# Performance work log

Measured on AMD Instinct MI355X. Metric: run time of the kernel, lower is better.

The kernel has to match this reference:

```python
import jax, jax.numpy as jnp
import numpy as np

IMG_SIZE = 1280
STRIDE = 4
NUM_CLASSES = 80
TOPK = 1000
NMS_THRESH = 0.6
SCALE_CLAMP = float(np.log(1000.0))  # DEFAULT_SCALE_CLAMP
N_ANCHORS = (IMG_SIZE // STRIDE) ** 2  # 102400


def _anchors():
    # generate_anchors: meshgrid over fmp, stacked as (x, y), flattened
    fmp = IMG_SIZE // STRIDE
    ys, xs = jnp.meshgrid(jnp.arange(fmp), jnp.arange(fmp), indexing='ij')
    return jnp.stack([xs, ys], axis=-1).reshape(-1, 2).astype(jnp.float32)


def _decode_boxes(anchors, reg):
    # [wl, ht, wr, hb] -> [x1, y1, x2, y2], scaled by stride
    reg = jnp.exp(jnp.minimum(reg, SCALE_CLAMP))
    xy1 = anchors - reg[..., :2]
    xy2 = anchors + reg[..., 2:]
    return jnp.concatenate([xy1, xy2], axis=-1) * STRIDE


def _iou_matrix(b):
    # pairwise IoU with the exact eps handling of the original numpy NMS
    x1, y1, x2, y2 = b[:, 0], b[:, 1], b[:, 2], b[:, 3]
    areas = (x2 - x1) * (y2 - y1)
    xx1 = jnp.maximum(x1[:, None], x1[None, :])
    yy1 = jnp.maximum(y1[:, None], y1[None, :])
    xx2 = jnp.minimum(x2[:, None], x2[None, :])
    yy2 = jnp.minimum(y2[:, None], y2[None, :])
    w = jnp.maximum(1e-10, xx2 - xx1)
    h = jnp.maximum(1e-10, yy2 - yy1)
    inter = w * h
    return inter / (areas[:, None] + areas[None, :] - inter + 1e-10)


def _greedy_nms(iou, same_class):
    # boxes are pre-sorted by score descending (top_k output order), so a
    # single greedy pass with a same-class mask is equivalent to the
    # original per-class loop (each class subset preserves score order).
    K = iou.shape[0]
    suppress = (iou > NMS_THRESH) & same_class
    idx = jnp.arange(K)

    def body(keep, i):
        row = suppress[i] & keep[i]  # only a kept box suppresses others
        keep = keep & ~(row & (idx > i))
        return keep, None

    keep0 = jnp.ones((K,), dtype=bool)
    keep, _ = jax.lax.scan(body, keep0, idx)
    return keep


def setup_inputs() -> dict:
    key = jax.random.key(0)
    k1, k2, k3 = jax.random.split(key, 3)
    hmp_pred = jax.random.normal(k1, (N_ANCHORS, NUM_CLASSES), dtype=jnp.float32)
    reg_pred = jax.random.normal(k2, (N_ANCHORS, 4), dtype=jnp.float32)
    iou_pred = jax.random.normal(k3, (N_ANCHORS, 1), dtype=jnp.float32)
    return {"hmp_pred": hmp_pred, "reg_pred": reg_pred, "iou_pred": iou_pred}


def reference(hmp_pred, reg_pred, iou_pred):
    # score fusion: sqrt(sigmoid(hmp) * sigmoid(iou)), max over classes
    fused = jnp.sqrt(jax.nn.sigmoid(hmp_pred) * jax.nn.sigmoid(iou_pred))  # [N, C]
    scores = jnp.max(fused, axis=-1)
    labels = jnp.argmax(fused, axis=-1)

    # top-k selection (sorted descending)
    scores, indices = jax.lax.top_k(scores, TOPK)
    labels = labels[indices]
    reg = reg_pred[indices]
    anc = _anchors()[indices]

    # decode + normalize + clamp
    bboxes = jnp.clip(_decode_boxes(anc, reg) / IMG_SIZE, 0.0, 1.0)  # [K, 4]

    # class-aware greedy NMS; keep mask replaces the dynamic-shape filter
    same_class = labels[:, None] == labels[None, :]
    keep = _greedy_nms(_iou_matrix(bboxes), same_class)
    return scores, labels, bboxes, keep
```

## Files before the change

kernel.cpp:

```cpp
#include <hip/hip_runtime.h>
#include <stdint.h>

#define N_ANCH 102400
#define FMP 320
#define K_TOP 1000
#define NMS_T 0.6f
#define SC_CLAMP 6.907755278982137f
#define IMGF 1280.0f
#define NBINS 16384

#define OFF_SCORES   0u
#define OFF_LABELS   409600u
#define OFF_HIST     819200u
#define OFF_META     884736u
#define OFF_KEYS     884992u
#define OFF_BOXES    917760u
#define OFF_LAB1K    933760u
#define OFF_MASK     937760u
#define OFF_DIAG     1065760u

__device__ __forceinline__ float sigf(float x) {
    return 1.0f / (1.0f + expf(-x));
}

__global__ __launch_bounds__(256) void k_scores(const float* __restrict__ hmp,
                                                const float* __restrict__ iou,
                                                float* __restrict__ scores,
                                                uint32_t* __restrict__ labels,
                                                uint32_t* __restrict__ hist,
                                                uint32_t* __restrict__ meta,
                                                uint64_t* __restrict__ diag) {
    int blk = blockIdx.x;
    if (blk < 64) {
        hist[blk * 256 + threadIdx.x] = 0u;
    } else if (blk == 64) {
        if (threadIdx.x < 64) meta[threadIdx.x] = 0u;
#pragma unroll
        for (int k = 0; k < 4; ++k) diag[threadIdx.x * 4 + k] = 0ull;
    }
    int gid = blk * 256 + threadIdx.x;
    int a = gid >> 2;
    int q = gid & 3;
    float si = sigf(iou[a]);
    const float4* row4 = (const float4*)hmp + (size_t)a * 20 + q;
    float4 v[5];
#pragma unroll
    for (int j = 0; j < 5; ++j) v[j] = row4[j * 4];
    float best = -1.0f;
    int bc = 0;
#pragma unroll
    for (int j = 0; j < 5; ++j) {
        int cb = j * 16 + q * 4;
        float f;
        f = sqrtf(sigf(v[j].x) * si); if (f > best) { best = f; bc = cb; }
        f = sqrtf(sigf(v[j].y) * si); if (f > best) { best = f; bc = cb + 1; }
        f = sqrtf(sigf(v[j].z) * si); if (f > best) { best = f; bc = cb + 2; }
        f = sqrtf(sigf(v[j].w) * si); if (f > best) { best = f; bc = cb + 3; }
    }
#pragma unroll
    for (int off = 1; off <= 2; off <<= 1) {
        float of = __shfl_xor(best, off);
        int   oc = __shfl_xor(bc, off);
        if (of > best || (of == best && oc < bc)) { best = of; bc = oc; }
    }
    if (q == 0) {
        scores[a] = best;
        labels[a] = (uint32_t)bc;
    }
}

__global__ __launch_bounds__(1024) void k_hist(const float* __restrict__ scores,
                                               uint32_t* __restrict__ hist,
                                               uint32_t* __restrict__ meta) {
    __shared__ uint32_t lh[NBINS];
    __shared__ int lastFlag;
    for (int i = threadIdx.x; i < NBINS; i += 1024) lh[i] = 0u;
    __syncthreads();
    int base = blockIdx.x * 1600;
    for (int k = threadIdx.x; k < 1600; k += 1024) {
        uint32_t bin = __float_as_uint(scores[base + k]) >> 16;
        atomicAdd(&lh[bin], 1u);
    }
    __syncthreads();
    for (int i = threadIdx.x; i < NBINS; i += 1024) {
        uint32_t c = lh[i];
        if (c) atomicAdd(&hist[i], c);
    }
    __threadfence();
    __syncthreads();
    if (threadIdx.x == 0) lastFlag = (atomicAdd(&meta[8], 1u) == 63u);
    __syncthreads();
    if (!lastFlag) return;
    __threadfence();
    int t = threadIdx.x;
    uint32_t s = 0;
#pragma unroll
    for (int b = 0; b < 16; ++b) s += hist[t * 16 + b];
    lh[t] = s;
    __syncthreads();
    for (int off = 1; off < 1024; off <<= 1) {
        uint32_t v = lh[t] + ((t + off < 1024) ? lh[t + off] : 0u);
        __syncthreads();
        lh[t] = v;
        __syncthreads();
    }
    uint32_t inc   = lh[t];
    uint32_t above = (t < 1023) ? lh[t + 1] : 0u;
    if (above < K_TOP && inc >= K_TOP) {
        uint32_t loc[16];
#pragma unroll
        for (int b = 0; b < 16; ++b) loc[b] = hist[t * 16 + b];
        uint32_t cnt = above;
        for (int b = 15; b >= 0; --b) {
            cnt += loc[b];
            if (cnt >= K_TOP) { meta[0] = (uint32_t)(t * 16 + b); break; }
        }
    }
}

__global__ __launch_bounds__(256) void k_collect(const float* __restrict__ scores,
                                                 uint32_t* __restrict__ meta,
                                                 uint64_t* __restrict__ keys) {
    __shared__ uint32_t cnt, base;
    if (threadIdx.x == 0) cnt = 0u;
    __syncthreads();
    int i = blockIdx.x * 256 + threadIdx.x;
    uint32_t bits = __float_as_uint(scores[i]);
    bool cand = (bits >> 16) >= meta[0];
    uint32_t pos = 0;
    if (cand) pos = atomicAdd(&cnt, 1u);
    __syncthreads();
    if (threadIdx.x == 0 && cnt) base = atomicAdd(&meta[2], cnt);
    __syncthreads();
    if (cand) {
        uint32_t p = base + pos;
        if (p < 4096u)
            keys[p] = ((uint64_t)bits << 32) | (uint64_t)(0xFFFFFFFFu - (uint32_t)i);
    }
}

__global__ __launch_bounds__(1024) void k_rank(const uint64_t* __restrict__ keys,
                                               const uint32_t* __restrict__ meta,
                                               const uint32_t* __restrict__ labels,
                                               const float* __restrict__ reg,
                                               float* __restrict__ out,
                                               float* __restrict__ boxes,
                                               uint32_t* __restrict__ lab1k) {
    __shared__ uint64_t sk[4096];
    uint32_t M = meta[2];
    if (M > 4096u) M = 4096u;
    if ((uint32_t)(blockIdx.x * 16) >= M) return;
    for (uint32_t i = threadIdx.x; i < M; i += 1024) sk[i] = keys[i];
    __syncthreads();
    int lane = threadIdx.x & 63;
    int wg = blockIdx.x * 16 + (threadIdx.x >> 6);
    if ((uint32_t)wg >= M) return;
    uint64_t mykey = sk[wg];
    uint32_t rank = 0;
    for (uint32_t j = lane; j < M; j += 64) rank += (sk[j] > mykey) ? 1u : 0u;
#pragma unroll
    for (int off = 32; off; off >>= 1) rank += __shfl_xor(rank, off);
    if (lane != 0 || rank >= K_TOP) return;
    int t = (int)rank;
    uint32_t sbits = (uint32_t)(mykey >> 32);
    uint32_t idx   = 0xFFFFFFFFu - (uint32_t)(mykey & 0xFFFFFFFFull);
    float score = __uint_as_float(sbits);
    uint32_t lab = labels[idx];
    out[t]         = score;
    out[K_TOP + t] = (float)lab;
    lab1k[t]       = lab;
    float ax = (float)(idx % FMP);
    float ay = (float)(idx / FMP);
    float4 rr = ((const float4*)reg)[idx];
    float e0 = expf(fminf(rr.x, SC_CLAMP));
    float e1 = expf(fminf(rr.y, SC_CLAMP));
    float e2 = expf(fminf(rr.z, SC_CLAMP));
    float e3 = expf(fminf(rr.w, SC_CLAMP));
    float x1 = fminf(fmaxf((ax - e0) * 4.0f / IMGF, 0.0f), 1.0f);
    float y1 = fminf(fmaxf((ay - e1) * 4.0f / IMGF, 0.0f), 1.0f);
    float x2 = fminf(fmaxf((ax + e2) * 4.0f / IMGF, 0.0f), 1.0f);
    float y2 = fminf(fmaxf((ay + e3) * 4.0f / IMGF, 0.0f), 1.0f);
    out[2 * K_TOP + t * 4 + 0] = x1;
    out[2 * K_TOP + t * 4 + 1] = y1;
    out[2 * K_TOP + t * 4 + 2] = x2;
    out[2 * K_TOP + t * 4 + 3] = y2;
    boxes[t * 4 + 0] = x1;
    boxes[t * 4 + 1] = y1;
    boxes[t * 4 + 2] = x2;
    boxes[t * 4 + 3] = y2;
}

__global__ __launch_bounds__(1024) void k_mask(const float* __restrict__ boxes,
                                               const uint32_t* __restrict__ lab1k,
                                               uint64_t* __restrict__ mask,
                                               uint64_t* __restrict__ diag) {
    int r = blockIdx.x * 16 + (threadIdx.x >> 6);
    int lane = threadIdx.x & 63;
    if (r >= K_TOP) return;
    float4 bi = ((const float4*)boxes)[r];
    uint32_t li = lab1k[r];
    float areai = (bi.z - bi.x) * (bi.w - bi.y);
    int iw = r >> 6;
    uint64_t dw = 0ull;
#pragma unroll
    for (int w = 0; w < 16; ++w) {
        int j = w * 64 + lane;
        bool sup = false;
        if (j < K_TOP && j > r) {
            float4 bj = ((const float4*)boxes)[j];
            float areaj = (bj.z - bj.x) * (bj.w - bj.y);
            float xx1 = fmaxf(bi.x, bj.x);
            float yy1 = fmaxf(bi.y, bj.y);
            float xx2 = fminf(bi.z, bj.z);
            float yy2 = fminf(bi.w, bj.w);
            float ww = fmaxf(1e-10f, xx2 - xx1);
            float hh = fmaxf(1e-10f, yy2 - yy1);
            float inter = ww * hh;
            float iouv = inter / (areai + areaj - inter + 1e-10f);
            sup = (iouv > NMS_T) && (li == lab1k[j]);
        }
        unsigned long long m = __ballot(sup);
        if (lane == 0) mask[(size_t)r * 16 + w] = (uint64_t)m;
        if (w == iw) dw = (uint64_t)m;
    }
    if (lane == 0) diag[r] = dw;
}

__global__ __launch_bounds__(64, 1) void k_scan(const uint64_t* __restrict__ mask,
                                                const uint64_t* __restrict__ diag,
                                                float* __restrict__ out) {
    int lane = threadIdx.x;
    int q = lane >> 4, wrd = lane & 15;
    uint64_t remv = 0ull;
    uint64_t dcur = diag[lane];
    for (int g = 0; g < 16; ++g) {
        uint64_t dnxt = (g < 15) ? diag[64 * (g + 1) + lane] : 0ull;
        uint64_t bun[16];
        if (g < 15) {
#pragma unroll
            for (int r4 = 0; r4 < 16; ++r4)
                bun[r4] = mask[(size_t)(64 * g + 4 * r4 + q) * 16 + wrd];
        }
        uint32_t dlo = 0, dhi = 0;
#pragma unroll
        for (int qq = 0; qq < 4; ++qq) {
            dlo |= __builtin_amdgcn_readlane((uint32_t)remv, qq * 16 + g);
            dhi |= __builtin_amdgcn_readlane((uint32_t)(remv >> 32), qq * 16 + g);
        }
        uint64_t D = ((uint64_t)dhi << 32) | dlo;
#pragma unroll
        for (int b = 0; b < 64; ++b) {
            uint32_t tlo = __builtin_amdgcn_readlane((uint32_t)dcur, b);
            uint32_t thi = __builtin_amdgcn_readlane((uint32_t)(dcur >> 32), b);
            uint64_t T = ((uint64_t)thi << 32) | tlo;
            uint64_t sel = ((D >> b) & 1ull) - 1ull;
            D |= T & sel;
        }
        uint64_t keepg = ~D;
        int j = g * 64 + lane;
        if (j < K_TOP) out[6 * K_TOP + j] = (float)((keepg >> lane) & 1ull);
        if (g < 15) {
#pragma unroll
            for (int r4 = 0; r4 < 16; ++r4) {
                uint32_t kb = (uint32_t)(keepg >> (4 * r4 + q)) & 1u;
                uint64_t mm = 0ull - (uint64_t)kb;
                remv |= bun[r4] & mm;
            }
        }
        dcur = dnxt;
    }
}

extern "C" void kernel_launch(void* const* d_in, const int* in_sizes, int n_in,
                              void* d_out, int out_size, void* d_ws, size_t ws_size,
                              hipStream_t stream) {
    const float* hmp = (const float*)d_in[0];
    const float* reg = (const float*)d_in[1];
    const float* iou = (const float*)d_in[2];
    float* out = (float*)d_out;
    char* ws = (char*)d_ws;

    float*    scores = (float*)(ws + OFF_SCORES);
    uint32_t* labels = (uint32_t*)(ws + OFF_LABELS);
    uint32_t* hist   = (uint32_t*)(ws + OFF_HIST);
    uint32_t* meta   = (uint32_t*)(ws + OFF_META);
    uint64_t* keys   = (uint64_t*)(ws + OFF_KEYS);
    float*    boxes  = (float*)(ws + OFF_BOXES);
    uint32_t* lab1k  = (uint32_t*)(ws + OFF_LAB1K);
    uint64_t* mask   = (uint64_t*)(ws + OFF_MASK);
    uint64_t* diag   = (uint64_t*)(ws + OFF_DIAG);

    k_scores<<<dim3(N_ANCH * 4 / 256), dim3(256), 0, stream>>>(hmp, iou, scores, labels, hist, meta, diag);
    k_hist<<<dim3(64), dim3(1024), 0, stream>>>(scores, hist, meta);
    k_collect<<<dim3(N_ANCH / 256), dim3(256), 0, stream>>>(scores, meta, keys);
    k_rank<<<dim3(256), dim3(1024), 0, stream>>>(keys, meta, labels, reg, out, boxes, lab1k);
    k_mask<<<dim3(63), dim3(1024), 0, stream>>>(boxes, lab1k, mask, diag);
    k_scan<<<dim3(1), dim3(64), 0, stream>>>(mask, diag, out);
}
```

Baseline: 156.5 us.

## Fuse histogram, collect, rank, mask and scan into one persistent kernel

Replaces five separate launches (histogram, candidate collect, rank/decode, IoU mask, greedy scan) with a single 100-block persistent kernel. The stages are separated by software grid barriers built on atomic counters in the meta area. Each block computes the score cutoff redundantly from the global histogram, which removes the last-block election step. This aims to cut kernel launch gaps and inter-kernel drain time, at the cost of spin-wait barriers that depend on all 100 blocks being resident at once.

```diff
diff --git a/kernel.cpp b/kernel.cpp
--- a/kernel.cpp
+++ b/kernel.cpp
@@ -8,6 +8,8 @@
 #define SC_CLAMP 6.907755278982137f
 #define IMGF 1280.0f
 #define NBINS 16384
+#define NBLK2 100
+#define NTHR2 1024
 
 #define OFF_SCORES   0u
 #define OFF_LABELS   409600u
@@ -21,6 +23,17 @@
 
 __device__ __forceinline__ float sigf(float x) {
     return 1.0f / (1.0f + expf(-x));
+}
+
+__device__ __forceinline__ void gbar(uint32_t* ctr, uint32_t target) {
+    __threadfence();
+    __syncthreads();
+    if (threadIdx.x == 0) {
+        atomicAdd(ctr, 1u);
+        while (atomicAdd(ctr, 0u) < target) __builtin_amdgcn_s_sleep(10);
+    }
+    __syncthreads();
+    __threadfence();
 }
 
 __global__ __launch_bounds__(256) void k_scores(const float* __restrict__ hmp,
@@ -69,205 +82,198 @@
     }
 }
 
-__global__ __launch_bounds__(1024) void k_hist(const float* __restrict__ scores,
-                                               uint32_t* __restrict__ hist,
-                                               uint32_t* __restrict__ meta) {
-    __shared__ uint32_t lh[NBINS];
-    __shared__ int lastFlag;
-    for (int i = threadIdx.x; i < NBINS; i += 1024) lh[i] = 0u;
-    __syncthreads();
-    int base = blockIdx.x * 1600;
-    for (int k = threadIdx.x; k < 1600; k += 1024) {
-        uint32_t bin = __float_as_uint(scores[base + k]) >> 16;
-        atomicAdd(&lh[bin], 1u);
-    }
-    __syncthreads();
-    for (int i = threadIdx.x; i < NBINS; i += 1024) {
-        uint32_t c = lh[i];
+__global__ __launch_bounds__(NTHR2, 4) void k_mega(const float* __restrict__ scores,
+                                                   const uint32_t* __restrict__ labels,
+                                                   const float* __restrict__ reg,
+                                                   uint32_t* __restrict__ hist,
+                                                   uint32_t* __restrict__ meta,
+                                                   uint64_t* __restrict__ keys,
+                                                   float* __restrict__ boxes,
+                                                   uint32_t* __restrict__ lab1k,
+                                                   uint64_t* __restrict__ mask,
+                                                   uint64_t* __restrict__ diag,
+                                                   float* __restrict__ out) {
+    __shared__ __align__(16) uint32_t sh32[NBINS];
+    uint64_t* sk = (uint64_t*)sh32;
+    const int tid  = threadIdx.x;
+    const int blk  = blockIdx.x;
+    const int gtid = blk * NTHR2 + tid;
+    const int lane = tid & 63;
+    const int wv   = tid >> 6;
+
+    for (int i = tid; i < NBINS; i += NTHR2) sh32[i] = 0u;
+    __syncthreads();
+    uint32_t mybits = __float_as_uint(scores[gtid]);
+    atomicAdd(&sh32[mybits >> 16], 1u);
+    __syncthreads();
+    for (int i = tid; i < NBINS; i += NTHR2) {
+        uint32_t c = sh32[i];
         if (c) atomicAdd(&hist[i], c);
     }
-    __threadfence();
-    __syncthreads();
-    if (threadIdx.x == 0) lastFlag = (atomicAdd(&meta[8], 1u) == 63u);
-    __syncthreads();
-    if (!lastFlag) return;
-    __threadfence();
-    int t = threadIdx.x;
-    uint32_t s = 0;
-#pragma unroll
-    for (int b = 0; b < 16; ++b) s += hist[t * 16 + b];
-    lh[t] = s;
-    __syncthreads();
-    for (int off = 1; off < 1024; off <<= 1) {
-        uint32_t v = lh[t] + ((t + off < 1024) ? lh[t + off] : 0u);
+    gbar(&meta[8], NBLK2);
+
+    {
+        uint32_t s = 0;
+#pragma unroll
+        for (int b = 0; b < 16; ++b) s += hist[tid * 16 + b];
+        sh32[tid] = s;
         __syncthreads();
-        lh[t] = v;
+        for (int off = 1; off < NTHR2; off <<= 1) {
+            uint32_t v = sh32[tid] + ((tid + off < NTHR2) ? sh32[tid + off] : 0u);
+            __syncthreads();
+            sh32[tid] = v;
+            __syncthreads();
+        }
+        uint32_t inc   = sh32[tid];
+        uint32_t above = (tid < NTHR2 - 1) ? sh32[tid + 1] : 0u;
+        if (above < K_TOP && inc >= K_TOP) {
+            uint32_t loc[16];
+#pragma unroll
+            for (int b = 0; b < 16; ++b) loc[b] = hist[tid * 16 + b];
+            uint32_t cnt = above;
+            for (int b = 15; b >= 0; --b) {
+                cnt += loc[b];
+                if (cnt >= K_TOP) { sh32[1025] = (uint32_t)(tid * 16 + b); break; }
+            }
+        }
         __syncthreads();
     }
-    uint32_t inc   = lh[t];
-    uint32_t above = (t < 1023) ? lh[t + 1] : 0u;
-    if (above < K_TOP && inc >= K_TOP) {
-        uint32_t loc[16];
-#pragma unroll
-        for (int b = 0; b < 16; ++b) loc[b] = hist[t * 16 + b];
-        uint32_t cnt = above;
-        for (int b = 15; b >= 0; --b) {
-            cnt += loc[b];
-            if (cnt >= K_TOP) { meta[0] = (uint32_t)(t * 16 + b); break; }
-        }
-    }
-}
-
-__global__ __launch_bounds__(256) void k_collect(const float* __restrict__ scores,
-                                                 uint32_t* __restrict__ meta,
-                                                 uint64_t* __restrict__ keys) {
-    __shared__ uint32_t cnt, base;
-    if (threadIdx.x == 0) cnt = 0u;
-    __syncthreads();
-    int i = blockIdx.x * 256 + threadIdx.x;
-    uint32_t bits = __float_as_uint(scores[i]);
-    bool cand = (bits >> 16) >= meta[0];
+    uint32_t cutoff = sh32[1025];
+    __syncthreads();
+
+    if (tid == 0) sh32[0] = 0u;
+    __syncthreads();
+    bool cand = (mybits >> 16) >= cutoff;
     uint32_t pos = 0;
-    if (cand) pos = atomicAdd(&cnt, 1u);
-    __syncthreads();
-    if (threadIdx.x == 0 && cnt) base = atomicAdd(&meta[2], cnt);
+    if (cand) pos = atomicAdd(&sh32[0], 1u);
+    __syncthreads();
+    if (tid == 0) sh32[1] = sh32[0] ? atomicAdd(&meta[2], sh32[0]) : 0u;
     __syncthreads();
     if (cand) {
-        uint32_t p = base + pos;
+        uint32_t p = sh32[1] + pos;
         if (p < 4096u)
-            keys[p] = ((uint64_t)bits << 32) | (uint64_t)(0xFFFFFFFFu - (uint32_t)i);
-    }
-}
-
-__global__ __launch_bounds__(1024) void k_rank(const uint64_t* __restrict__ keys,
-                                               const uint32_t* __restrict__ meta,
-                                               const uint32_t* __restrict__ labels,
-                                               const float* __restrict__ reg,
-                                               float* __restrict__ out,
-                                               float* __restrict__ boxes,
-                                               uint32_t* __restrict__ lab1k) {
-    __shared__ uint64_t sk[4096];
-    uint32_t M = meta[2];
-    if (M > 4096u) M = 4096u;
-    if ((uint32_t)(blockIdx.x * 16) >= M) return;
-    for (uint32_t i = threadIdx.x; i < M; i += 1024) sk[i] = keys[i];
-    __syncthreads();
-    int lane = threadIdx.x & 63;
-    int wg = blockIdx.x * 16 + (threadIdx.x >> 6);
-    if ((uint32_t)wg >= M) return;
-    uint64_t mykey = sk[wg];
-    uint32_t rank = 0;
-    for (uint32_t j = lane; j < M; j += 64) rank += (sk[j] > mykey) ? 1u : 0u;
-#pragma unroll
-    for (int off = 32; off; off >>= 1) rank += __shfl_xor(rank, off);
-    if (lane != 0 || rank >= K_TOP) return;
-    int t = (int)rank;
-    uint32_t sbits = (uint32_t)(mykey >> 32);
-    uint32_t idx   = 0xFFFFFFFFu - (uint32_t)(mykey & 0xFFFFFFFFull);
-    float score = __uint_as_float(sbits);
-    uint32_t lab = labels[idx];
-    out[t]         = score;
-    out[K_TOP + t] = (float)lab;
-    lab1k[t]       = lab;
-    float ax = (float)(idx % FMP);
-    float ay = (float)(idx / FMP);
-    float4 rr = ((const float4*)reg)[idx];
-    float e0 = expf(fminf(rr.x, SC_CLAMP));
-    float e1 = expf(fminf(rr.y, SC_CLAMP));
-    float e2 = expf(fminf(rr.z, SC_CLAMP));
-    float e3 = expf(fminf(rr.w, SC_CLAMP));
-    float x1 = fminf(fmaxf((ax - e0) * 4.0f / IMGF, 0.0f), 1.0f);
-    float y1 = fminf(fmaxf((ay - e1) * 4.0f / IMGF, 0.0f), 1.0f);
-    float x2 = fminf(fmaxf((ax + e2) * 4.0f / IMGF, 0.0f), 1.0f);
-    float y2 = fminf(fmaxf((ay + e3) * 4.0f / IMGF, 0.0f), 1.0f);
-    out[2 * K_TOP + t * 4 + 0] = x1;
-    out[2 * K_TOP + t * 4 + 1] = y1;
-    out[2 * K_TOP + t * 4 + 2] = x2;
-    out[2 * K_TOP + t * 4 + 3] = y2;
-    boxes[t * 4 + 0] = x1;
-    boxes[t * 4 + 1] = y1;
-    boxes[t * 4 + 2] = x2;
-    boxes[t * 4 + 3] = y2;
-}
-
-__global__ __launch_bounds__(1024) void k_mask(const float* __restrict__ boxes,
-                                               const uint32_t* __restrict__ lab1k,
-                                               uint64_t* __restrict__ mask,
-                                               uint64_t* __restrict__ diag) {
-    int r = blockIdx.x * 16 + (threadIdx.x >> 6);
-    int lane = threadIdx.x & 63;
-    if (r >= K_TOP) return;
-    float4 bi = ((const float4*)boxes)[r];
-    uint32_t li = lab1k[r];
-    float areai = (bi.z - bi.x) * (bi.w - bi.y);
-    int iw = r >> 6;
-    uint64_t dw = 0ull;
-#pragma unroll
-    for (int w = 0; w < 16; ++w) {
-        int j = w * 64 + lane;
-        bool sup = false;
-        if (j < K_TOP && j > r) {
-            float4 bj = ((const float4*)boxes)[j];
-            float areaj = (bj.z - bj.x) * (bj.w - bj.y);
-            float xx1 = fmaxf(bi.x, bj.x);
-            float yy1 = fmaxf(bi.y, bj.y);
-            float xx2 = fminf(bi.z, bj.z);
-            float yy2 = fminf(bi.w, bj.w);
-            float ww = fmaxf(1e-10f, xx2 - xx1);
-            float hh = fmaxf(1e-10f, yy2 - yy1);
-            float inter = ww * hh;
-            float iouv = inter / (areai + areaj - inter + 1e-10f);
-            sup = (iouv > NMS_T) && (li == lab1k[j]);
-        }
-        unsigned long long m = __ballot(sup);
-        if (lane == 0) mask[(size_t)r * 16 + w] = (uint64_t)m;
-        if (w == iw) dw = (uint64_t)m;
-    }
-    if (lane == 0) diag[r] = dw;
-}
-
-__global__ __launch_bounds__(64, 1) void k_scan(const uint64_t* __restrict__ mask,
-                                                const uint64_t* __restrict__ diag,
-                                                float* __restrict__ out) {
-    int lane = threadIdx.x;
-    int q = lane >> 4, wrd = lane & 15;
-    uint64_t remv = 0ull;
-    uint64_t dcur = diag[lane];
-    for (int g = 0; g < 16; ++g) {
-        uint64_t dnxt = (g < 15) ? diag[64 * (g + 1) + lane] : 0ull;
-        uint64_t bun[16];
-        if (g < 15) {
-#pragma unroll
-            for (int r4 = 0; r4 < 16; ++r4)
-                bun[r4] = mask[(size_t)(64 * g + 4 * r4 + q) * 16 + wrd];
-        }
-        uint32_t dlo = 0, dhi = 0;
-#pragma unroll
-        for (int qq = 0; qq < 4; ++qq) {
-            dlo |= __builtin_amdgcn_readlane((uint32_t)remv, qq * 16 + g);
-            dhi |= __builtin_amdgcn_readlane((uint32_t)(remv >> 32), qq * 16 + g);
-        }
-        uint64_t D = ((uint64_t)dhi << 32) | dlo;
-#pragma unroll
-        for (int b = 0; b < 64; ++b) {
-            uint32_t tlo = __builtin_amdgcn_readlane((uint32_t)dcur, b);
-            uint32_t thi = __builtin_amdgcn_readlane((uint32_t)(dcur >> 32), b);
-            uint64_t T = ((uint64_t)thi << 32) | tlo;
-            uint64_t sel = ((D >> b) & 1ull) - 1ull;
-            D |= T & sel;
-        }
-        uint64_t keepg = ~D;
-        int j = g * 64 + lane;
-        if (j < K_TOP) out[6 * K_TOP + j] = (float)((keepg >> lane) & 1ull);
-        if (g < 15) {
-#pragma unroll
-            for (int r4 = 0; r4 < 16; ++r4) {
-                uint32_t kb = (uint32_t)(keepg >> (4 * r4 + q)) & 1u;
-                uint64_t mm = 0ull - (uint64_t)kb;
-                remv |= bun[r4] & mm;
-            }
-        }
-        dcur = dnxt;
+            keys[p] = ((uint64_t)mybits << 32) | (uint64_t)(0xFFFFFFFFu - (uint32_t)gtid);
+    }
+    gbar(&meta[9], NBLK2);
+
+    {
+        uint32_t M = meta[2];
+        if (M > 4096u) M = 4096u;
+        for (uint32_t i = tid; i < M; i += NTHR2) sk[i] = keys[i];
+        __syncthreads();
+        for (uint32_t wg = (uint32_t)(blk * 16 + wv); wg < M; wg += NBLK2 * 16) {
+            uint64_t mykey = sk[wg];
+            uint32_t rank = 0;
+            for (uint32_t j = lane; j < M; j += 64) rank += (sk[j] > mykey) ? 1u : 0u;
+#pragma unroll
+            for (int off = 32; off; off >>= 1) rank += __shfl_xor(rank, off);
+            if (lane == 0 && rank < K_TOP) {
+                int t = (int)rank;
+                uint32_t sbits = (uint32_t)(mykey >> 32);
+                uint32_t idx   = 0xFFFFFFFFu - (uint32_t)(mykey & 0xFFFFFFFFull);
+                float score = __uint_as_float(sbits);
+                uint32_t lab = labels[idx];
+                out[t]         = score;
+                out[K_TOP + t] = (float)lab;
+                lab1k[t]       = lab;
+                float ax = (float)(idx % FMP);
+                float ay = (float)(idx / FMP);
+                float4 rr = ((const float4*)reg)[idx];
+                float e0 = expf(fminf(rr.x, SC_CLAMP));
+                float e1 = expf(fminf(rr.y, SC_CLAMP));
+                float e2 = expf(fminf(rr.z, SC_CLAMP));
+                float e3 = expf(fminf(rr.w, SC_CLAMP));
+                float x1 = fminf(fmaxf((ax - e0) * 4.0f / IMGF, 0.0f), 1.0f);
+                float y1 = fminf(fmaxf((ay - e1) * 4.0f / IMGF, 0.0f), 1.0f);
+                float x2 = fminf(fmaxf((ax + e2) * 4.0f / IMGF, 0.0f), 1.0f);
+                float y2 = fminf(fmaxf((ay + e3) * 4.0f / IMGF, 0.0f), 1.0f);
+                out[2 * K_TOP + t * 4 + 0] = x1;
+                out[2 * K_TOP + t * 4 + 1] = y1;
+                out[2 * K_TOP + t * 4 + 2] = x2;
+                out[2 * K_TOP + t * 4 + 3] = y2;
+                boxes[t * 4 + 0] = x1;
+                boxes[t * 4 + 1] = y1;
+                boxes[t * 4 + 2] = x2;
+                boxes[t * 4 + 3] = y2;
+            }
+        }
+    }
+    gbar(&meta[10], NBLK2);
+
+    {
+        int r = blk * 16 + wv;
+        if (r < K_TOP) {
+            float4 bi = ((const float4*)boxes)[r];
+            uint32_t li = lab1k[r];
+            float areai = (bi.z - bi.x) * (bi.w - bi.y);
+            int iw = r >> 6;
+            uint64_t dw = 0ull;
+#pragma unroll
+            for (int w = 0; w < 16; ++w) {
+                int j = w * 64 + lane;
+                bool sup = false;
+                if (j < K_TOP && j > r) {
+                    float4 bj = ((const float4*)boxes)[j];
+                    float areaj = (bj.z - bj.x) * (bj.w - bj.y);
+                    float xx1 = fmaxf(bi.x, bj.x);
+                    float yy1 = fmaxf(bi.y, bj.y);
+                    float xx2 = fminf(bi.z, bj.z);
+                    float yy2 = fminf(bi.w, bj.w);
+                    float ww = fmaxf(1e-10f, xx2 - xx1);
+                    float hh = fmaxf(1e-10f, yy2 - yy1);
+                    float inter = ww * hh;
+                    float iouv = inter / (areai + areaj - inter + 1e-10f);
+                    sup = (iouv > NMS_T) && (li == lab1k[j]);
+                }
+                unsigned long long m = __ballot(sup);
+                if (lane == 0) mask[(size_t)r * 16 + w] = (uint64_t)m;
+                if (w == iw) dw = (uint64_t)m;
+            }
+            if (lane == 0) diag[r] = dw;
+        }
+    }
+    gbar(&meta[11], NBLK2);
+
+    if (blk == 0 && tid < 64) {
+        int q = lane >> 4, wrd = lane & 15;
+        uint64_t remv = 0ull;
+        uint64_t dcur = diag[lane];
+        for (int g = 0; g < 16; ++g) {
+            uint64_t dnxt = (g < 15) ? diag[64 * (g + 1) + lane] : 0ull;
+            uint64_t bun[16];
+            if (g < 15) {
+#pragma unroll
+                for (int r4 = 0; r4 < 16; ++r4)
+                    bun[r4] = mask[(size_t)(64 * g + 4 * r4 + q) * 16 + wrd];
+            }
+            uint32_t dlo = 0, dhi = 0;
+#pragma unroll
+            for (int qq = 0; qq < 4; ++qq) {
+                dlo |= __builtin_amdgcn_readlane((uint32_t)remv, qq * 16 + g);
+                dhi |= __builtin_amdgcn_readlane((uint32_t)(remv >> 32), qq * 16 + g);
+            }
+            uint64_t D = ((uint64_t)dhi << 32) | dlo;
+#pragma unroll
+            for (int b = 0; b < 64; ++b) {
+                uint32_t tlo = __builtin_amdgcn_readlane((uint32_t)dcur, b);
+                uint32_t thi = __builtin_amdgcn_readlane((uint32_t)(dcur >> 32), b);
+                uint64_t T = ((uint64_t)thi << 32) | tlo;
+                uint64_t sel = ((D >> b) & 1ull) - 1ull;
+                D |= T & sel;
+            }
+            uint64_t keepg = ~D;
+            int j = g * 64 + lane;
+            if (j < K_TOP) out[6 * K_TOP + j] = (float)((keepg >> lane) & 1ull);
+            if (g < 15) {
+#pragma unroll
+                for (int r4 = 0; r4 < 16; ++r4) {
+                    uint32_t kb = (uint32_t)(keepg >> (4 * r4 + q)) & 1u;
+                    uint64_t mm = 0ull - (uint64_t)kb;
+                    remv |= bun[r4] & mm;
+                }
+            }
+            dcur = dnxt;
+        }
     }
 }
 
@@ -291,9 +297,6 @@
     uint64_t* diag   = (uint64_t*)(ws + OFF_DIAG);
 
     k_scores<<<dim3(N_ANCH * 4 / 256), dim3(256), 0, stream>>>(hmp, iou, scores, labels, hist, meta, diag);
-    k_hist<<<dim3(64), dim3(1024), 0, stream>>>(scores, hist, meta);
-    k_collect<<<dim3(N_ANCH / 256), dim3(256), 0, stream>>>(scores, meta, keys);
-    k_rank<<<dim3(256), dim3(1024), 0, stream>>>(keys, meta, labels, reg, out, boxes, lab1k);
-    k_mask<<<dim3(63), dim3(1024), 0, stream>>>(boxes, lab1k, mask, diag);
-    k_scan<<<dim3(1), dim3(64), 0, stream>>>(mask, diag, out);
-}
+    k_mega<<<dim3(NBLK2), dim3(NTHR2), 0, stream>>>(scores, labels, reg, hist, meta,
+                                                    keys, boxes, lab1k, mask, diag, out);
+}
```

Result: slower. 338.8 us (+116.5%).

## Fuse threshold, candidate collection and ranking into last histogram block

Applied to the files above, without the earlier changes.

The histogram kernel's last-finishing block now computes the cutoff, rescans all 102400 scores to gather candidates into shared memory, and ranks them there, replacing the separate collect and rank kernels. This removes two kernel launches and the global keys round trip. In exchange, the collection scan and the O(M^2) ranking run on a single 1024-thread block instead of being spread across hundreds of blocks, so serial work on one CU increases.

```diff
diff --git a/kernel.cpp b/kernel.cpp
--- a/kernel.cpp
+++ b/kernel.cpp
@@ -13,7 +13,6 @@
 #define OFF_LABELS   409600u
 #define OFF_HIST     819200u
 #define OFF_META     884736u
-#define OFF_KEYS     884992u
 #define OFF_BOXES    917760u
 #define OFF_LAB1K    933760u
 #define OFF_MASK     937760u
@@ -70,124 +69,117 @@
 }
 
 __global__ __launch_bounds__(1024) void k_hist(const float* __restrict__ scores,
-                                               uint32_t* __restrict__ hist,
-                                               uint32_t* __restrict__ meta) {
-    __shared__ uint32_t lh[NBINS];
-    __shared__ int lastFlag;
-    for (int i = threadIdx.x; i < NBINS; i += 1024) lh[i] = 0u;
-    __syncthreads();
-    int base = blockIdx.x * 1600;
-    for (int k = threadIdx.x; k < 1600; k += 1024) {
-        uint32_t bin = __float_as_uint(scores[base + k]) >> 16;
-        atomicAdd(&lh[bin], 1u);
-    }
-    __syncthreads();
-    for (int i = threadIdx.x; i < NBINS; i += 1024) {
-        uint32_t c = lh[i];
-        if (c) atomicAdd(&hist[i], c);
-    }
-    __threadfence();
-    __syncthreads();
-    if (threadIdx.x == 0) lastFlag = (atomicAdd(&meta[8], 1u) == 63u);
-    __syncthreads();
-    if (!lastFlag) return;
-    __threadfence();
-    int t = threadIdx.x;
-    uint32_t s = 0;
-#pragma unroll
-    for (int b = 0; b < 16; ++b) s += hist[t * 16 + b];
-    lh[t] = s;
-    __syncthreads();
-    for (int off = 1; off < 1024; off <<= 1) {
-        uint32_t v = lh[t] + ((t + off < 1024) ? lh[t + off] : 0u);
-        __syncthreads();
-        lh[t] = v;
-        __syncthreads();
-    }
-    uint32_t inc   = lh[t];
-    uint32_t above = (t < 1023) ? lh[t + 1] : 0u;
-    if (above < K_TOP && inc >= K_TOP) {
-        uint32_t loc[16];
-#pragma unroll
-        for (int b = 0; b < 16; ++b) loc[b] = hist[t * 16 + b];
-        uint32_t cnt = above;
-        for (int b = 15; b >= 0; --b) {
-            cnt += loc[b];
-            if (cnt >= K_TOP) { meta[0] = (uint32_t)(t * 16 + b); break; }
-        }
-    }
-}
-
-__global__ __launch_bounds__(256) void k_collect(const float* __restrict__ scores,
-                                                 uint32_t* __restrict__ meta,
-                                                 uint64_t* __restrict__ keys) {
-    __shared__ uint32_t cnt, base;
-    if (threadIdx.x == 0) cnt = 0u;
-    __syncthreads();
-    int i = blockIdx.x * 256 + threadIdx.x;
-    uint32_t bits = __float_as_uint(scores[i]);
-    bool cand = (bits >> 16) >= meta[0];
-    uint32_t pos = 0;
-    if (cand) pos = atomicAdd(&cnt, 1u);
-    __syncthreads();
-    if (threadIdx.x == 0 && cnt) base = atomicAdd(&meta[2], cnt);
-    __syncthreads();
-    if (cand) {
-        uint32_t p = base + pos;
-        if (p < 4096u)
-            keys[p] = ((uint64_t)bits << 32) | (uint64_t)(0xFFFFFFFFu - (uint32_t)i);
-    }
-}
-
-__global__ __launch_bounds__(1024) void k_rank(const uint64_t* __restrict__ keys,
-                                               const uint32_t* __restrict__ meta,
                                                const uint32_t* __restrict__ labels,
                                                const float* __restrict__ reg,
+                                               uint32_t* __restrict__ hist,
+                                               uint32_t* __restrict__ meta,
                                                float* __restrict__ out,
                                                float* __restrict__ boxes,
                                                uint32_t* __restrict__ lab1k) {
-    __shared__ uint64_t sk[4096];
-    uint32_t M = meta[2];
+    __shared__ __align__(16) uint32_t lh[NBINS];
+    __shared__ int lastFlag;
+    __shared__ uint32_t s_cut, s_cnt;
+    const int t = threadIdx.x;
+
+    for (int i = t; i < NBINS; i += 1024) lh[i] = 0u;
+    __syncthreads();
+    int base = blockIdx.x * 1600;
+    for (int k = t; k < 1600; k += 1024)
+        atomicAdd(&lh[__float_as_uint(scores[base + k]) >> 16], 1u);
+    __syncthreads();
+    for (int i = t; i < NBINS; i += 1024) {
+        uint32_t c = lh[i];
+        if (c) atomicAdd(&hist[i], c);
+    }
+    __threadfence();
+    __syncthreads();
+    if (t == 0) lastFlag = (atomicAdd(&meta[8], 1u) == 63u);
+    __syncthreads();
+    if (!lastFlag) return;
+    __threadfence();
+
+    {
+        uint32_t s = 0;
+#pragma unroll
+        for (int b = 0; b < 16; ++b) s += hist[t * 16 + b];
+        lh[t] = s;
+        __syncthreads();
+        for (int off = 1; off < 1024; off <<= 1) {
+            uint32_t v = lh[t] + ((t + off < 1024) ? lh[t + off] : 0u);
+            __syncthreads();
+            lh[t] = v;
+            __syncthreads();
+        }
+        uint32_t inc   = lh[t];
+        uint32_t above = (t < 1023) ? lh[t + 1] : 0u;
+        if (above < K_TOP && inc >= K_TOP) {
+            uint32_t loc[16];
+#pragma unroll
+            for (int b = 0; b < 16; ++b) loc[b] = hist[t * 16 + b];
+            uint32_t cnt = above;
+            for (int b = 15; b >= 0; --b) {
+                cnt += loc[b];
+                if (cnt >= K_TOP) { s_cut = (uint32_t)(t * 16 + b); break; }
+            }
+        }
+        __syncthreads();
+    }
+    uint32_t cutoff = s_cut;
+    __syncthreads();
+
+    uint64_t* sk = (uint64_t*)lh;
+    if (t == 0) s_cnt = 0u;
+    __syncthreads();
+    for (int k = t; k < N_ANCH; k += 1024) {
+        uint32_t bits = __float_as_uint(scores[k]);
+        if ((bits >> 16) >= cutoff) {
+            uint32_t p = atomicAdd(&s_cnt, 1u);
+            if (p < 4096u)
+                sk[p] = ((uint64_t)bits << 32) | (uint64_t)(0xFFFFFFFFu - (uint32_t)k);
+        }
+    }
+    __syncthreads();
+    uint32_t M = s_cnt;
     if (M > 4096u) M = 4096u;
-    if ((uint32_t)(blockIdx.x * 16) >= M) return;
-    for (uint32_t i = threadIdx.x; i < M; i += 1024) sk[i] = keys[i];
-    __syncthreads();
-    int lane = threadIdx.x & 63;
-    int wg = blockIdx.x * 16 + (threadIdx.x >> 6);
-    if ((uint32_t)wg >= M) return;
-    uint64_t mykey = sk[wg];
-    uint32_t rank = 0;
-    for (uint32_t j = lane; j < M; j += 64) rank += (sk[j] > mykey) ? 1u : 0u;
-#pragma unroll
-    for (int off = 32; off; off >>= 1) rank += __shfl_xor(rank, off);
-    if (lane != 0 || rank >= K_TOP) return;
-    int t = (int)rank;
-    uint32_t sbits = (uint32_t)(mykey >> 32);
-    uint32_t idx   = 0xFFFFFFFFu - (uint32_t)(mykey & 0xFFFFFFFFull);
-    float score = __uint_as_float(sbits);
-    uint32_t lab = labels[idx];
-    out[t]         = score;
-    out[K_TOP + t] = (float)lab;
-    lab1k[t]       = lab;
-    float ax = (float)(idx % FMP);
-    float ay = (float)(idx / FMP);
-    float4 rr = ((const float4*)reg)[idx];
-    float e0 = expf(fminf(rr.x, SC_CLAMP));
-    float e1 = expf(fminf(rr.y, SC_CLAMP));
-    float e2 = expf(fminf(rr.z, SC_CLAMP));
-    float e3 = expf(fminf(rr.w, SC_CLAMP));
-    float x1 = fminf(fmaxf((ax - e0) * 4.0f / IMGF, 0.0f), 1.0f);
-    float y1 = fminf(fmaxf((ay - e1) * 4.0f / IMGF, 0.0f), 1.0f);
-    float x2 = fminf(fmaxf((ax + e2) * 4.0f / IMGF, 0.0f), 1.0f);
-    float y2 = fminf(fmaxf((ay + e3) * 4.0f / IMGF, 0.0f), 1.0f);
-    out[2 * K_TOP + t * 4 + 0] = x1;
-    out[2 * K_TOP + t * 4 + 1] = y1;
-    out[2 * K_TOP + t * 4 + 2] = x2;
-    out[2 * K_TOP + t * 4 + 3] = y2;
-    boxes[t * 4 + 0] = x1;
-    boxes[t * 4 + 1] = y1;
-    boxes[t * 4 + 2] = x2;
-    boxes[t * 4 + 3] = y2;
+
+    for (uint32_t c = t; c < M; c += 1024) {
+        uint64_t mykey = sk[c];
+        uint32_t rank = 0;
+        uint32_t j = 0;
+        for (; j + 4 <= M; j += 4) {
+#pragma unroll
+            for (int u = 0; u < 4; ++u) rank += (sk[j + u] > mykey) ? 1u : 0u;
+        }
+        for (; j < M; ++j) rank += (sk[j] > mykey) ? 1u : 0u;
+        if (rank >= K_TOP) continue;
+        int r = (int)rank;
+        uint32_t sbits = (uint32_t)(mykey >> 32);
+        uint32_t idx   = 0xFFFFFFFFu - (uint32_t)(mykey & 0xFFFFFFFFull);
+        float score = __uint_as_float(sbits);
+        uint32_t lab = labels[idx];
+        out[r]         = score;
+        out[K_TOP + r] = (float)lab;
+        lab1k[r]       = lab;
+        float ax = (float)(idx % FMP);
+        float ay = (float)(idx / FMP);
+        float4 rr = ((const float4*)reg)[idx];
+        float e0 = expf(fminf(rr.x, SC_CLAMP));
+        float e1 = expf(fminf(rr.y, SC_CLAMP));
+        float e2 = expf(fminf(rr.z, SC_CLAMP));
+        float e3 = expf(fminf(rr.w, SC_CLAMP));
+        float x1 = fminf(fmaxf((ax - e0) * 4.0f / IMGF, 0.0f), 1.0f);
+        float y1 = fminf(fmaxf((ay - e1) * 4.0f / IMGF, 0.0f), 1.0f);
+        float x2 = fminf(fmaxf((ax + e2) * 4.0f / IMGF, 0.0f), 1.0f);
+        float y2 = fminf(fmaxf((ay + e3) * 4.0f / IMGF, 0.0f), 1.0f);
+        out[2 * K_TOP + r * 4 + 0] = x1;
+        out[2 * K_TOP + r * 4 + 1] = y1;
+        out[2 * K_TOP + r * 4 + 2] = x2;
+        out[2 * K_TOP + r * 4 + 3] = y2;
+        boxes[r * 4 + 0] = x1;
+        boxes[r * 4 + 1] = y1;
+        boxes[r * 4 + 2] = x2;
+        boxes[r * 4 + 3] = y2;
+    }
 }
 
 __global__ __launch_bounds__(1024) void k_mask(const float* __restrict__ boxes,
@@ -284,16 +276,13 @@
     uint32_t* labels = (uint32_t*)(ws + OFF_LABELS);
     uint32_t* hist   = (uint32_t*)(ws + OFF_HIST);
     uint32_t* meta   = (uint32_t*)(ws + OFF_META);
-    uint64_t* keys   = (uint64_t*)(ws + OFF_KEYS);
     float*    boxes  = (float*)(ws + OFF_BOXES);
     uint32_t* lab1k  = (uint32_t*)(ws + OFF_LAB1K);
     uint64_t* mask   = (uint64_t*)(ws + OFF_MASK);
     uint64_t* diag   = (uint64_t*)(ws + OFF_DIAG);
 
     k_scores<<<dim3(N_ANCH * 4 / 256), dim3(256), 0, stream>>>(hmp, iou, scores, labels, hist, meta, diag);
-    k_hist<<<dim3(64), dim3(1024), 0, stream>>>(scores, hist, meta);
-    k_collect<<<dim3(N_ANCH / 256), dim3(256), 0, stream>>>(scores, meta, keys);
-    k_rank<<<dim3(256), dim3(1024), 0, stream>>>(keys, meta, labels, reg, out, boxes, lab1k);
+    k_hist<<<dim3(64), dim3(1024), 0, stream>>>(scores, labels, reg, hist, meta, out, boxes, lab1k);
     k_mask<<<dim3(63), dim3(1024), 0, stream>>>(boxes, lab1k, mask, diag);
     k_scan<<<dim3(1), dim3(64), 0, stream>>>(mask, diag, out);
 }
```

After: 224.8 us. +43.6%, slower.
